# Optimization experiments

Hardware: AMD Instinct MI355X
Metric: run time of the kernel (lower is better)

Reference implementation:

```python
import jax, jax.numpy as jnp
import numpy as np

EMBED_DIM = 1024
NUM_HEADS = 16
HEAD_DIM = EMBED_DIM // NUM_HEADS
SCALING = HEAD_DIM ** -0.5


def setup_inputs() -> dict:
    key = jax.random.key(0)
    k1, k2, k3, k4, k5 = jax.random.split(key, 5)
    B, S, E, H = 2, 2048, EMBED_DIM, NUM_HEADS
    x = jax.random.normal(k1, (B, S, E), dtype=jnp.float32)
    # nn.Linear weights: [out_features, in_features]
    W_A = jax.random.normal(k2, (H, E), dtype=jnp.float32) * (E ** -0.5)
    W_V = jax.random.normal(k3, (E, E), dtype=jnp.float32) * (E ** -0.5)
    W_O = jax.random.normal(k4, (E, E), dtype=jnp.float32) * (E ** -0.5)
    b_O = jax.random.normal(k5, (E,), dtype=jnp.float32) * 0.01
    return {"x": x, "W_A": W_A, "W_V": W_V, "W_O": W_O, "b_O": b_O}


def reference(x, W_A, W_V, W_O, b_O):
    B, S, E = x.shape
    H, D = NUM_HEADS, HEAD_DIM
    # per-head scalar attention logits, softmax over sequence dim
    z = jnp.einsum('bse,he->bsh', x, W_A) * SCALING          # [B,S,H]
    z = jax.nn.softmax(z, axis=1)                            # softmax over seq
    zp = jnp.transpose(z, (0, 2, 1))                         # [B,H,S]
    # causal roll matrix: roll[b,h,i,j] = z[b,h,i-j] for j<=i else 0
    i = jnp.arange(S)[:, None]
    j = jnp.arange(S)[None, :]
    idx = (i - j) % S                                        # [S,S]
    tril = (j <= i).astype(x.dtype)                          # causal mask
    roll = zp[:, :, idx] * tril                              # [B,H,S,S]
    # values split into heads
    v = jnp.einsum('bse,fe->bsf', x, W_V).reshape(B, S, H, D)  # [B,S,H,D]
    out = jnp.einsum('bhij,bjhd->bihd', roll, v).reshape(B, S, E)
    return jnp.einsum('bse,fe->bsf', out, W_O) + b_O
```

## Files before the change

kernel.cpp:

```cpp
#include <hip/hip_runtime.h>
#include <hip/hip_bf16.h>
#include <stdint.h>

typedef unsigned short u16;
typedef short short8 __attribute__((ext_vector_type(8)));
typedef float f32x4 __attribute__((ext_vector_type(4)));

#define SEQ 2048
#define EMB 1024
#define NH 16
#define HD 64
#define ZP 2112

__device__ inline u16 f2bf(float f) {
    uint32_t u = __builtin_bit_cast(uint32_t, f);
    uint32_t r = (u + 0x7FFFu + ((u >> 16) & 1u)) >> 16;
    return (u16)r;
}

__device__ inline void gload16(const void* g, void* l) {
    __builtin_amdgcn_global_load_lds(
        (const __attribute__((address_space(1))) void*)g,
        (__attribute__((address_space(3))) void*)l, 16, 0, 0);
}

__global__ __launch_bounds__(256) void cast_kernel(const float* __restrict__ src,
                                                   u16* __restrict__ dst, int n4) {
    int i = blockIdx.x * 256 + threadIdx.x;
    if (i < n4) {
        float4 f = reinterpret_cast<const float4*>(src)[i];
        union { u16 u[4]; uint2 v; } o;
        o.u[0] = f2bf(f.x); o.u[1] = f2bf(f.y); o.u[2] = f2bf(f.z); o.u[3] = f2bf(f.w);
        reinterpret_cast<uint2*>(dst)[i] = o.v;
    }
}

__global__ __launch_bounds__(256) void cast2_kernel(const float* __restrict__ s0,
                                                    u16* __restrict__ d0,
                                                    const float* __restrict__ s1,
                                                    u16* __restrict__ d1, int n4each) {
    int i = blockIdx.x * 256 + threadIdx.x;
    const float* src = (i < n4each) ? s0 : s1;
    u16* dst = (i < n4each) ? d0 : d1;
    int j = (i < n4each) ? i : i - n4each;
    float4 f = reinterpret_cast<const float4*>(src)[j];
    union { u16 u[4]; uint2 v; } o;
    o.u[0] = f2bf(f.x); o.u[1] = f2bf(f.y); o.u[2] = f2bf(f.z); o.u[3] = f2bf(f.w);
    reinterpret_cast<uint2*>(dst)[j] = o.v;
}

__global__ __launch_bounds__(256) void logits_kernel(const float* __restrict__ x,
                                                     const float* __restrict__ W_A,
                                                     float* __restrict__ zl) {
    __shared__ float wa[NH * EMB];
    int t = threadIdx.x;
    for (int i = t; i < NH * EMB / 4; i += 256)
        reinterpret_cast<float4*>(wa)[i] = reinterpret_cast<const float4*>(W_A)[i];
    __syncthreads();
    int w = t >> 6, l = t & 63;
    int row0 = blockIdx.x * 16 + w * 4;
    for (int rr = 0; rr < 4; rr++) {
        int gs = row0 + rr;
        int b = gs >> 11, s = gs & 2047;
        const float* xr = x + (size_t)gs * EMB;
        float xv[16];
#pragma unroll
        for (int q = 0; q < 16; q++) xv[q] = xr[l + 64 * q];
#pragma unroll
        for (int h = 0; h < NH; h++) {
            float a = 0.f;
#pragma unroll
            for (int q = 0; q < 16; q++) a += xv[q] * wa[h * EMB + l + 64 * q];
#pragma unroll
            for (int off = 32; off; off >>= 1) a += __shfl_xor(a, off);
            if (l == h) zl[((size_t)b * NH + h) * SEQ + s] = a * 0.125f;
        }
    }
}

__global__ __launch_bounds__(256) void softmax_kernel(const float* __restrict__ zl,
                                                      u16* __restrict__ zr) {
    int bh = blockIdx.x;
    const float* src = zl + (size_t)bh * SEQ;
    int t = threadIdx.x;
    int w = t >> 6, l = t & 63;
    __shared__ float red[4];
    __shared__ float bc;
    float v[8];
#pragma unroll
    for (int q = 0; q < 8; q++) v[q] = src[t + 256 * q];
    float m = v[0];
#pragma unroll
    for (int q = 1; q < 8; q++) m = fmaxf(m, v[q]);
#pragma unroll
    for (int off = 32; off; off >>= 1) m = fmaxf(m, __shfl_xor(m, off));
    if (l == 0) red[w] = m;
    __syncthreads();
    if (t == 0) bc = fmaxf(fmaxf(red[0], red[1]), fmaxf(red[2], red[3]));
    __syncthreads();
    m = bc;
    float s = 0.f;
#pragma unroll
    for (int q = 0; q < 8; q++) { v[q] = expf(v[q] - m); s += v[q]; }
#pragma unroll
    for (int off = 32; off; off >>= 1) s += __shfl_xor(s, off);
    if (l == 0) red[w] = s;
    __syncthreads();
    if (t == 0) bc = red[0] + red[1] + red[2] + red[3];
    __syncthreads();
    float inv = 1.0f / bc;
#pragma unroll
    for (int q = 0; q < 8; q++) {
        int sidx = t + 256 * q;
        zr[(size_t)bh * ZP + (SEQ - 1 - sidx)] = f2bf(v[q] * inv);
    }
    if (t < ZP - SEQ) zr[(size_t)bh * ZP + SEQ + t] = 0;
}

template <int OUTMODE>
__global__ __launch_bounds__(512) void gemm_bt(const u16* __restrict__ A,
                                               const u16* __restrict__ Bw,
                                               u16* __restrict__ Cb, float* __restrict__ Cf,
                                               const float* __restrict__ bias,
                                               int M, int N, int K) {
    __shared__ u16 As[2][128 * 64];
    __shared__ u16 Bs[2][128 * 64];
    const int t = threadIdx.x;
    const int m0 = blockIdx.y * 128, n0 = blockIdx.x * 128;
    const int w = t >> 6, l = t & 63;
    const int wr = w >> 2, wc = w & 3;
    const int lrow = l & 15, lk = l >> 4;
    const int r7 = lrow & 7;

    const int srow = w * 16 + (l >> 3);
    const int scb = ((l & 7) ^ (l >> 3)) * 8;
    const u16* gA0 = A + (size_t)(m0 + srow) * K + scb;
    const u16* gA1 = gA0 + (size_t)8 * K;
    const u16* gB0 = Bw + (size_t)(n0 + srow) * K + scb;
    const u16* gB1 = gB0 + (size_t)8 * K;
    const int ldsbase = w * 16 * 64;

    f32x4 acc[4][2];
#pragma unroll
    for (int i = 0; i < 4; i++)
#pragma unroll
        for (int j = 0; j < 2; j++) acc[i][j] = (f32x4){0.f, 0.f, 0.f, 0.f};

    const int NT = K >> 6;
    gload16(gA0, &As[0][ldsbase]);
    gload16(gA1, &As[0][ldsbase + 512]);
    gload16(gB0, &Bs[0][ldsbase]);
    gload16(gB1, &Bs[0][ldsbase + 512]);
    __syncthreads();

    for (int kt = 0; kt < NT; kt++) {
        const int cur = kt & 1;
        if (kt + 1 < NT) {
            const int k0 = (kt + 1) * 64;
            gload16(gA0 + k0, &As[cur ^ 1][ldsbase]);
            gload16(gA1 + k0, &As[cur ^ 1][ldsbase + 512]);
            gload16(gB0 + k0, &Bs[cur ^ 1][ldsbase]);
            gload16(gB1 + k0, &Bs[cur ^ 1][ldsbase + 512]);
        }
#pragma unroll
        for (int kk = 0; kk < 2; kk++) {
            const int cs = ((kk * 4 + lk) ^ r7) * 8;
            short8 af[4], bf2[2];
#pragma unroll
            for (int mi = 0; mi < 4; mi++)
                af[mi] = *reinterpret_cast<const short8*>(
                    &As[cur][(wr * 64 + mi * 16 + lrow) * 64 + cs]);
#pragma unroll
            for (int ni = 0; ni < 2; ni++)
                bf2[ni] = *reinterpret_cast<const short8*>(
                    &Bs[cur][(wc * 32 + ni * 16 + lrow) * 64 + cs]);
#pragma unroll
            for (int mi = 0; mi < 4; mi++)
#pragma unroll
                for (int ni = 0; ni < 2; ni++)
                    acc[mi][ni] = __builtin_amdgcn_mfma_f32_16x16x32_bf16(af[mi], bf2[ni], acc[mi][ni], 0, 0, 0);
        }
        __syncthreads();
    }
#pragma unroll
    for (int mi = 0; mi < 4; mi++)
#pragma unroll
        for (int ni = 0; ni < 2; ni++)
#pragma unroll
            for (int r = 0; r < 4; r++) {
                int row = m0 + wr * 64 + mi * 16 + (l >> 4) * 4 + r;
                int col = n0 + wc * 32 + ni * 16 + lrow;
                if constexpr (OUTMODE == 0)
                    Cb[(size_t)row * N + col] = f2bf(acc[mi][ni][r]);
                else
                    Cf[(size_t)row * N + col] = acc[mi][ni][r] + bias[col];
            }
}

__global__ __launch_bounds__(256) void conv_kernel(const u16* __restrict__ zr,
                                                   const u16* __restrict__ vt2,
                                                   u16* __restrict__ cv) {
    const int bh = blockIdx.y;
    const int b = bh >> 4, h = bh & 15;
    __shared__ uint zsl[2176];
    const int t = threadIdx.x;
    {
        const uint* zp = reinterpret_cast<const uint*>(zr + (size_t)bh * ZP);
        for (int i = t; i < 1088; i += 256) {
            uint v0 = (i < 1056) ? zp[i] : 0u;
            uint v1 = (i < 1055) ? zp[i + 1] : 0u;
            zsl[i] = v0;
            zsl[1088 + i] = (v0 >> 16) | (v1 << 16);
        }
    }
    __syncthreads();

    const int w = t >> 6, l = t & 63;
    const int taskid = blockIdx.x * 4 + w;
    const int pp = taskid >> 1;
    const int ch = taskid & 1;
    const int lrow = l & 15;
    const int lk8 = (l >> 4) * 8;
    const int col0 = ch * 32;
    const int ebase = h * 64 + col0;
    const size_t boff = (size_t)b * SEQ;

    int slices[2] = {pp, 31 - pp};
#pragma unroll 1
    for (int si = 0; si < 2; si++) {
        const int s = slices[si];
        const int row0 = s * 64;
        const int nk = 2 * s + 2;
        f32x4 acc[4][2];
#pragma unroll
        for (int i = 0; i < 4; i++)
#pragma unroll
            for (int j = 0; j < 2; j++) acc[i][j] = (f32x4){0.f, 0.f, 0.f, 0.f};

        union U { uint d[4]; short8 s8; };
        U b0[2], b1[2], a0[4], a1[4];

        const int obase = 2047 - row0 - lrow + lk8;

        auto loadB = [&](int k0, U* bf) {
#pragma unroll
            for (int ni = 0; ni < 2; ni++) {
                const u16* p = vt2 + (((size_t)(ebase + ni * 16 + lrow)) << 12) + boff + k0 + lk8;
                *reinterpret_cast<uint4*>(bf[ni].d) = *reinterpret_cast<const uint4*>(p);
            }
        };
        auto loadA = [&](int k0, U* af) {
#pragma unroll
            for (int mi = 0; mi < 4; mi++) {
                int o = obase - mi * 16 + k0;
                uint adw = (uint)(o >> 1) + (uint)((o & 1) * 1088);
#pragma unroll
                for (int q = 0; q < 4; q++) af[mi].d[q] = zsl[adw + q];
            }
        };

        loadB(0, b0);
        for (int k0 = 0; k0 < nk * 32; k0 += 64) {
            loadB(k0 + 32, b1);
            loadA(k0, a0);
#pragma unroll
            for (int mi = 0; mi < 4; mi++)
#pragma unroll
                for (int ni = 0; ni < 2; ni++)
                    acc[mi][ni] = __builtin_amdgcn_mfma_f32_16x16x32_bf16(a0[mi].s8, b0[ni].s8, acc[mi][ni], 0, 0, 0);
            if (k0 + 64 < nk * 32) loadB(k0 + 64, b0);
            loadA(k0 + 32, a1);
#pragma unroll
            for (int mi = 0; mi < 4; mi++)
#pragma unroll
                for (int ni = 0; ni < 2; ni++)
                    acc[mi][ni] = __builtin_amdgcn_mfma_f32_16x16x32_bf16(a1[mi].s8, b1[ni].s8, acc[mi][ni], 0, 0, 0);
        }
#pragma unroll
        for (int mi = 0; mi < 4; mi++)
#pragma unroll
            for (int ni = 0; ni < 2; ni++)
#pragma unroll
                for (int r = 0; r < 4; r++) {
                    int row = row0 + mi * 16 + (l >> 4) * 4 + r;
                    int col = col0 + ni * 16 + lrow;
                    cv[((size_t)b * SEQ + row) * EMB + h * 64 + col] = f2bf(acc[mi][ni][r]);
                }
    }
}

extern "C" void kernel_launch(void* const* d_in, const int* in_sizes, int n_in,
                              void* d_out, int out_size, void* d_ws, size_t ws_size,
                              hipStream_t stream) {
    const float* x   = (const float*)d_in[0];
    const float* W_A = (const float*)d_in[1];
    const float* W_V = (const float*)d_in[2];
    const float* W_O = (const float*)d_in[3];
    const float* b_O = (const float*)d_in[4];

    char* ws = (char*)d_ws;
    u16*   xb  = (u16*)(ws + 0);
    u16*   wvb = (u16*)(ws + 8388608);
    u16*   wob = (u16*)(ws + 10485760);
    float* zl  = (float*)(ws + 12582912);
    u16*   zr  = (u16*)(ws + 12845056);
    u16*   vt2 = (u16*)(ws + 12980224);
    u16*   cv  = (u16*)(ws + 21368832);

    cast_kernel<<<4096, 256, 0, stream>>>(x, xb, 1048576);
    cast2_kernel<<<2048, 256, 0, stream>>>(W_V, wvb, W_O, wob, 262144);
    logits_kernel<<<256, 256, 0, stream>>>(x, W_A, zl);
    softmax_kernel<<<32, 256, 0, stream>>>(zl, zr);
    gemm_bt<0><<<dim3(32, 8), 512, 0, stream>>>(wvb, xb, vt2, nullptr, nullptr, 1024, 4096, 1024);
    conv_kernel<<<dim3(8, 32), 256, 0, stream>>>(zr, vt2, cv);
    gemm_bt<1><<<dim3(8, 32), 512, 0, stream>>>(cv, wob, nullptr, (float*)d_out, b_O, 4096, 1024, 1024);
}
```

Before: 103.5 us.

## Merge casts, fold softmax into V GEMM, shrink GEMM tiles, split conv finer

Merges the three cast launches into one kernel and folds the softmax blocks into the V-projection GEMM launch as extra blocks. Both GEMMs move from 128x128 tiles with 512 threads to 128x64 tiles with 256 threads, which doubles the block count, and blocks are remapped so consecutive blocks share input tiles across XCDs. The causal conv kernel now uses 32-row slices paired for load balance, giving 512 blocks instead of 256, with a reworked double-buffered inner loop that handles an odd slice count. The aim is fewer launches and better CU occupancy on the small grids, at the cost of less reuse per tile and some heterogeneous blocks.

```diff
diff --git a/kernel.cpp b/kernel.cpp
--- a/kernel.cpp
+++ b/kernel.cpp
@@ -24,25 +24,22 @@
         (__attribute__((address_space(3))) void*)l, 16, 0, 0);
 }
 
-__global__ __launch_bounds__(256) void cast_kernel(const float* __restrict__ src,
-                                                   u16* __restrict__ dst, int n4) {
-    int i = blockIdx.x * 256 + threadIdx.x;
-    if (i < n4) {
-        float4 f = reinterpret_cast<const float4*>(src)[i];
-        union { u16 u[4]; uint2 v; } o;
-        o.u[0] = f2bf(f.x); o.u[1] = f2bf(f.y); o.u[2] = f2bf(f.z); o.u[3] = f2bf(f.w);
-        reinterpret_cast<uint2*>(dst)[i] = o.v;
-    }
-}
-
-__global__ __launch_bounds__(256) void cast2_kernel(const float* __restrict__ s0,
-                                                    u16* __restrict__ d0,
-                                                    const float* __restrict__ s1,
-                                                    u16* __restrict__ d1, int n4each) {
-    int i = blockIdx.x * 256 + threadIdx.x;
-    const float* src = (i < n4each) ? s0 : s1;
-    u16* dst = (i < n4each) ? d0 : d1;
-    int j = (i < n4each) ? i : i - n4each;
+__global__ __launch_bounds__(256) void cast_all(const float* __restrict__ x,
+                                                const float* __restrict__ W_V,
+                                                const float* __restrict__ W_O,
+                                                u16* __restrict__ xb,
+                                                u16* __restrict__ wvb,
+                                                u16* __restrict__ wob) {
+    int bid = blockIdx.x, t = threadIdx.x;
+    const float* src;
+    u16* dst;
+    int j;
+    if (bid < 4096) { j = bid * 256 + t; src = x; dst = xb; }
+    else {
+        j = (bid - 4096) * 256 + t;
+        if (j < 262144) { src = W_V; dst = wvb; }
+        else { j -= 262144; src = W_O; dst = wob; }
+    }
     float4 f = reinterpret_cast<const float4*>(src)[j];
     union { u16 u[4]; uint2 v; } o;
     o.u[0] = f2bf(f.x); o.u[1] = f2bf(f.y); o.u[2] = f2bf(f.z); o.u[3] = f2bf(f.w);
@@ -78,9 +75,7 @@
     }
 }
 
-__global__ __launch_bounds__(256) void softmax_kernel(const float* __restrict__ zl,
-                                                      u16* __restrict__ zr) {
-    int bh = blockIdx.x;
+__device__ void softmax_body(const float* __restrict__ zl, u16* __restrict__ zr, int bh) {
     const float* src = zl + (size_t)bh * SEQ;
     int t = threadIdx.x;
     int w = t >> 6, l = t & 63;
@@ -117,50 +112,58 @@
     if (t < ZP - SEQ) zr[(size_t)bh * ZP + SEQ + t] = 0;
 }
 
-template <int OUTMODE>
-__global__ __launch_bounds__(512) void gemm_bt(const u16* __restrict__ A,
-                                               const u16* __restrict__ Bw,
-                                               u16* __restrict__ Cb, float* __restrict__ Cf,
-                                               const float* __restrict__ bias,
-                                               int M, int N, int K) {
+template <int OUTMODE, int MAP, bool SM>
+__global__ __launch_bounds__(256) void gemm64(const u16* __restrict__ A,
+                                              const u16* __restrict__ Bw,
+                                              u16* __restrict__ Cb, float* __restrict__ Cf,
+                                              const float* __restrict__ bias,
+                                              int M, int N, int K,
+                                              const float* __restrict__ zl,
+                                              u16* __restrict__ zr) {
+    if constexpr (SM) {
+        if (blockIdx.x >= 512) { softmax_body(zl, zr, blockIdx.x - 512); return; }
+    }
     __shared__ u16 As[2][128 * 64];
-    __shared__ u16 Bs[2][128 * 64];
+    __shared__ u16 Bs[2][64 * 64];
     const int t = threadIdx.x;
-    const int m0 = blockIdx.y * 128, n0 = blockIdx.x * 128;
+    const int i = blockIdx.x;
+    int xg, yg;
+    if constexpr (MAP == 0) { xg = (i & 7) * 8 + ((i >> 3) & 7); yg = i >> 6; }
+    else                    { yg = (i & 7) * 4 + ((i >> 3) & 3); xg = i >> 5; }
+    const int m0 = yg * 128, n0 = xg * 64;
     const int w = t >> 6, l = t & 63;
-    const int wr = w >> 2, wc = w & 3;
+    const int wr = w >> 1, wc = w & 1;
     const int lrow = l & 15, lk = l >> 4;
     const int r7 = lrow & 7;
 
-    const int srow = w * 16 + (l >> 3);
-    const int scb = ((l & 7) ^ (l >> 3)) * 8;
-    const u16* gA0 = A + (size_t)(m0 + srow) * K + scb;
-    const u16* gA1 = gA0 + (size_t)8 * K;
-    const u16* gB0 = Bw + (size_t)(n0 + srow) * K + scb;
-    const u16* gB1 = gB0 + (size_t)8 * K;
-    const int ldsbase = w * 16 * 64;
+    const int srow = t >> 3;
+    const int scb = ((t & 7) ^ ((t >> 3) & 7)) * 8;
+    const u16* gA = A + (size_t)(m0 + srow) * K + scb;
+    const u16* gB = Bw + (size_t)(n0 + srow) * K + scb;
+    const int ldst = w * 512;
 
     f32x4 acc[4][2];
 #pragma unroll
-    for (int i = 0; i < 4; i++)
-#pragma unroll
-        for (int j = 0; j < 2; j++) acc[i][j] = (f32x4){0.f, 0.f, 0.f, 0.f};
+    for (int a = 0; a < 4; a++)
+#pragma unroll
+        for (int b = 0; b < 2; b++) acc[a][b] = (f32x4){0.f, 0.f, 0.f, 0.f};
 
     const int NT = K >> 6;
-    gload16(gA0, &As[0][ldsbase]);
-    gload16(gA1, &As[0][ldsbase + 512]);
-    gload16(gB0, &Bs[0][ldsbase]);
-    gload16(gB1, &Bs[0][ldsbase + 512]);
+    const size_t rk32 = (size_t)32 * K;
+#pragma unroll
+    for (int c = 0; c < 4; c++) gload16(gA + c * rk32, &As[0][ldst + 2048 * c]);
+#pragma unroll
+    for (int c = 0; c < 2; c++) gload16(gB + c * rk32, &Bs[0][ldst + 2048 * c]);
     __syncthreads();
 
     for (int kt = 0; kt < NT; kt++) {
         const int cur = kt & 1;
         if (kt + 1 < NT) {
             const int k0 = (kt + 1) * 64;
-            gload16(gA0 + k0, &As[cur ^ 1][ldsbase]);
-            gload16(gA1 + k0, &As[cur ^ 1][ldsbase + 512]);
-            gload16(gB0 + k0, &Bs[cur ^ 1][ldsbase]);
-            gload16(gB1 + k0, &Bs[cur ^ 1][ldsbase + 512]);
+#pragma unroll
+            for (int c = 0; c < 4; c++) gload16(gA + k0 + c * rk32, &As[cur ^ 1][ldst + 2048 * c]);
+#pragma unroll
+            for (int c = 0; c < 2; c++) gload16(gB + k0 + c * rk32, &Bs[cur ^ 1][ldst + 2048 * c]);
         }
 #pragma unroll
         for (int kk = 0; kk < 2; kk++) {
@@ -188,7 +191,7 @@
         for (int ni = 0; ni < 2; ni++)
 #pragma unroll
             for (int r = 0; r < 4; r++) {
-                int row = m0 + wr * 64 + mi * 16 + (l >> 4) * 4 + r;
+                int row = m0 + wr * 64 + mi * 16 + lk * 4 + r;
                 int col = n0 + wc * 32 + ni * 16 + lrow;
                 if constexpr (OUTMODE == 0)
                     Cb[(size_t)row * N + col] = f2bf(acc[mi][ni][r]);
@@ -200,45 +203,46 @@
 __global__ __launch_bounds__(256) void conv_kernel(const u16* __restrict__ zr,
                                                    const u16* __restrict__ vt2,
                                                    u16* __restrict__ cv) {
-    const int bh = blockIdx.y;
+    const int i = blockIdx.x;
+    const int bh = (i & 7) * 4 + ((i >> 3) & 3);
+    const int rest = i >> 5;
     const int b = bh >> 4, h = bh & 15;
     __shared__ uint zsl[2176];
     const int t = threadIdx.x;
     {
         const uint* zp = reinterpret_cast<const uint*>(zr + (size_t)bh * ZP);
-        for (int i = t; i < 1088; i += 256) {
-            uint v0 = (i < 1056) ? zp[i] : 0u;
-            uint v1 = (i < 1055) ? zp[i + 1] : 0u;
-            zsl[i] = v0;
-            zsl[1088 + i] = (v0 >> 16) | (v1 << 16);
+        for (int q = t; q < 1088; q += 256) {
+            uint v0 = (q < 1056) ? zp[q] : 0u;
+            uint v1 = (q < 1055) ? zp[q + 1] : 0u;
+            zsl[q] = v0;
+            zsl[1088 + q] = (v0 >> 16) | (v1 << 16);
         }
     }
     __syncthreads();
 
     const int w = t >> 6, l = t & 63;
-    const int taskid = blockIdx.x * 4 + w;
-    const int pp = taskid >> 1;
-    const int ch = taskid & 1;
+    const int task = rest * 4 + w;
+    const int pp = task >> 1;
+    const int ch = task & 1;
     const int lrow = l & 15;
     const int lk8 = (l >> 4) * 8;
     const int col0 = ch * 32;
     const int ebase = h * 64 + col0;
     const size_t boff = (size_t)b * SEQ;
 
-    int slices[2] = {pp, 31 - pp};
+    union U { uint d[4]; short8 s8; };
+
+    int slices[2] = {pp, 63 - pp};
 #pragma unroll 1
     for (int si = 0; si < 2; si++) {
         const int s = slices[si];
-        const int row0 = s * 64;
-        const int nk = 2 * s + 2;
-        f32x4 acc[4][2];
-#pragma unroll
-        for (int i = 0; i < 4; i++)
-#pragma unroll
-            for (int j = 0; j < 2; j++) acc[i][j] = (f32x4){0.f, 0.f, 0.f, 0.f};
-
-        union U { uint d[4]; short8 s8; };
-        U b0[2], b1[2], a0[4], a1[4];
+        const int row0 = s * 32;
+        const int nk = s + 1;
+        f32x4 acc[2][2];
+#pragma unroll
+        for (int a = 0; a < 2; a++)
+#pragma unroll
+            for (int c = 0; c < 2; c++) acc[a][c] = (f32x4){0.f, 0.f, 0.f, 0.f};
 
         const int obase = 2047 - row0 - lrow + lk8;
 
@@ -251,7 +255,7 @@
         };
         auto loadA = [&](int k0, U* af) {
 #pragma unroll
-            for (int mi = 0; mi < 4; mi++) {
+            for (int mi = 0; mi < 2; mi++) {
                 int o = obase - mi * 16 + k0;
                 uint adw = (uint)(o >> 1) + (uint)((o & 1) * 1088);
 #pragma unroll
@@ -259,25 +263,36 @@
             }
         };
 
+        U a0[2], a1[2], b0[2], b1[2];
         loadB(0, b0);
-        for (int k0 = 0; k0 < nk * 32; k0 += 64) {
-            loadB(k0 + 32, b1);
-            loadA(k0, a0);
-#pragma unroll
-            for (int mi = 0; mi < 4; mi++)
+        loadB(32, b1);
+        loadA(0, a0);
+        int k = 0;
+        for (; k + 1 < nk; k += 2) {
+            loadA((k + 1) * 32, a1);
+#pragma unroll
+            for (int mi = 0; mi < 2; mi++)
 #pragma unroll
                 for (int ni = 0; ni < 2; ni++)
                     acc[mi][ni] = __builtin_amdgcn_mfma_f32_16x16x32_bf16(a0[mi].s8, b0[ni].s8, acc[mi][ni], 0, 0, 0);
-            if (k0 + 64 < nk * 32) loadB(k0 + 64, b0);
-            loadA(k0 + 32, a1);
-#pragma unroll
-            for (int mi = 0; mi < 4; mi++)
+            if (k + 2 < nk) loadB((k + 2) * 32, b0);
+            loadA((k + 2) * 32, a0);
+#pragma unroll
+            for (int mi = 0; mi < 2; mi++)
 #pragma unroll
                 for (int ni = 0; ni < 2; ni++)
                     acc[mi][ni] = __builtin_amdgcn_mfma_f32_16x16x32_bf16(a1[mi].s8, b1[ni].s8, acc[mi][ni], 0, 0, 0);
-        }
-#pragma unroll
-        for (int mi = 0; mi < 4; mi++)
+            if (k + 3 < nk) loadB((k + 3) * 32, b1);
+        }
+        if (nk & 1) {
+#pragma unroll
+            for (int mi = 0; mi < 2; mi++)
+#pragma unroll
+                for (int ni = 0; ni < 2; ni++)
+                    acc[mi][ni] = __builtin_amdgcn_mfma_f32_16x16x32_bf16(a0[mi].s8, b0[ni].s8, acc[mi][ni], 0, 0, 0);
+        }
+#pragma unroll
+        for (int mi = 0; mi < 2; mi++)
 #pragma unroll
             for (int ni = 0; ni < 2; ni++)
 #pragma unroll
@@ -307,11 +322,11 @@
     u16*   vt2 = (u16*)(ws + 12980224);
     u16*   cv  = (u16*)(ws + 21368832);
 
-    cast_kernel<<<4096, 256, 0, stream>>>(x, xb, 1048576);
-    cast2_kernel<<<2048, 256, 0, stream>>>(W_V, wvb, W_O, wob, 262144);
+    cast_all<<<6144, 256, 0, stream>>>(x, W_V, W_O, xb, wvb, wob);
     logits_kernel<<<256, 256, 0, stream>>>(x, W_A, zl);
-    softmax_kernel<<<32, 256, 0, stream>>>(zl, zr);
-    gemm_bt<0><<<dim3(32, 8), 512, 0, stream>>>(wvb, xb, vt2, nullptr, nullptr, 1024, 4096, 1024);
-    conv_kernel<<<dim3(8, 32), 256, 0, stream>>>(zr, vt2, cv);
-    gemm_bt<1><<<dim3(8, 32), 512, 0, stream>>>(cv, wob, nullptr, (float*)d_out, b_O, 4096, 1024, 1024);
-}
+    gemm64<0, 0, true><<<544, 256, 0, stream>>>(wvb, xb, vt2, nullptr, nullptr,
+                                                1024, 4096, 1024, zl, zr);
+    conv_kernel<<<512, 256, 0, stream>>>(zr, vt2, cv);
+    gemm64<1, 1, false><<<512, 256, 0, stream>>>(cv, wob, nullptr, (float*)d_out, b_O,
+                                                 4096, 1024, 1024, nullptr, nullptr);
+}
```

Result: no change. 103.1 us (-0.4%).
